# Kernel optimization log

Measured on AMD Instinct MI355X. Metric: run time of the kernel, lower is better.

## Reference

```python
import jax, jax.numpy as jnp
import numpy as np

N = 50000      # nodes
E = 1600000    # edges (before self loops)
F = 128        # input_dim
H = 4          # num_heads
D = 32         # hidden_dim (per head)
B = 16         # graphs in batch
NEG_SLOPE = 0.2  # PyG GATv2Conv default negative_slope


def setup_inputs() -> dict:
    key = jax.random.key(0)
    ks = jax.random.split(key, 8)
    x = jax.random.normal(ks[0], (N, F), dtype=jnp.float32)
    edge_index = jax.random.randint(ks[1], (2, E), 0, N, dtype=jnp.int32)
    batch = jnp.sort(jax.random.randint(ks[2], (N,), 0, B, dtype=jnp.int32))
    s = 0.05
    W_l = jax.random.normal(ks[3], (F, H * D), dtype=jnp.float32) * s
    b_l = jnp.zeros((H * D,), dtype=jnp.float32)
    W_r = jax.random.normal(ks[4], (F, H * D), dtype=jnp.float32) * s
    b_r = jnp.zeros((H * D,), dtype=jnp.float32)
    att = jax.random.normal(ks[5], (H, D), dtype=jnp.float32) * s
    bias = jnp.zeros((H * D,), dtype=jnp.float32)
    return {"x": x, "edge_index": edge_index, "batch": batch,
            "W_l": W_l, "b_l": b_l, "W_r": W_r, "b_r": b_r,
            "att": att, "bias": bias}


def reference(x, edge_index, batch, W_l, b_l, W_r, b_r, att, bias):
    n = x.shape[0]
    # PyG GATv2Conv adds self loops by default
    loops = jnp.arange(n, dtype=edge_index.dtype)
    src = jnp.concatenate([edge_index[0], loops])  # message source j
    dst = jnp.concatenate([edge_index[1], loops])  # message target i

    xl = (x @ W_l + b_l).reshape(n, H, D)  # source transform
    xr = (x @ W_r + b_r).reshape(n, H, D)  # target transform

    # per-edge GATv2 attention logits: a^T LeakyReLU(xl_j + xr_i)
    m = xl[src] + xr[dst]                                   # [E+N, H, D]
    e = jnp.sum(jax.nn.leaky_relu(m, NEG_SLOPE) * att, -1)  # [E+N, H]

    # softmax over incoming edges of each destination node
    e_max = jax.ops.segment_max(e, dst, num_segments=n)
    ex = jnp.exp(e - e_max[dst])
    den = jax.ops.segment_sum(ex, dst, num_segments=n)
    alpha = ex / den[dst]                                   # [E+N, H]

    # weighted scatter-sum aggregation of source features
    out = jax.ops.segment_sum(alpha[..., None] * xl[src], dst, num_segments=n)
    out = out.reshape(n, H * D) + bias                      # concat heads + bias
    out = jax.nn.relu(out)

    # global max pool over nodes of each graph
    pooled = jax.ops.segment_max(out, batch, num_segments=B)
    pooled = jnp.where(jnp.isfinite(pooled), pooled, 0.0)   # guard empty graphs
    return pooled
```

## Files before the change

kernel.cpp:

```cpp
#include <hip/hip_runtime.h>

#define NN 50000
#define NE 1600000
#define FDIM 128
#define CDIM 128
#define NGRAPH 16
#define SLOPE 0.2f
#define CSTRIDE 96
#define BINSH 7
#define NBIN 391
#define EPB 6400
#define NB1 250
#define EPT 25
#define CAP 5120
#define POOL_NODES 64
#define POOL_NB ((NN + POOL_NODES - 1) / POOL_NODES)
#define TNB 782

__device__ __forceinline__ unsigned short f2bf(float f) {
    unsigned u = __float_as_uint(f);
    return (unsigned short)((u + 0x7FFFu + ((u >> 16) & 1u)) >> 16);
}
__device__ __forceinline__ unsigned packbf(float a, float b) {
    return (unsigned)f2bf(a) | ((unsigned)f2bf(b) << 16);
}
#define BFLO(u) __uint_as_float((u) << 16)
#define BFHI(u) __uint_as_float((u) & 0xffff0000u)

typedef __attribute__((ext_vector_type(8))) short short8;
typedef __attribute__((ext_vector_type(4))) float f32x4;
union FragU { uint4 u; short8 s; };

__global__ __launch_bounds__(256) void k_init(float* __restrict__ out,
                                              int* __restrict__ gbin_cnt) {
    int i = blockIdx.x * 256 + threadIdx.x;
    if (i < NGRAPH * CDIM) out[i] = 0.f;
    if (i < NBIN) gbin_cnt[i] = 0;
}

__global__ __launch_bounds__(256) void k_transform(
    const float* __restrict__ x,
    const float* __restrict__ Wl, const float* __restrict__ bl,
    const float* __restrict__ Wr, const float* __restrict__ br,
    unsigned short* __restrict__ xlh, float* __restrict__ xr) {
    __shared__ uint4 wfrag[2048];
    const int tid   = threadIdx.x;
    const int wv    = tid >> 6;
    const int lane  = tid & 63;
    const int quad  = lane >> 4;
    const int col   = lane & 15;
    const int node0 = blockIdx.x * 64;
    const int nodeA = node0 + wv * 16 + col;
    const bool aval = nodeA < NN;

    FragU afrag[4];
#pragma unroll
    for (int kq = 0; kq < 4; kq++) {
        float4 lo = make_float4(0.f,0.f,0.f,0.f), hi = lo;
        if (aval) {
            const float* ap = &x[(size_t)nodeA * FDIM + kq * 32 + quad * 8];
            lo = *(const float4*)ap;
            hi = *(const float4*)(ap + 4);
        }
        afrag[kq].u.x = packbf(lo.x, lo.y);
        afrag[kq].u.y = packbf(lo.z, lo.w);
        afrag[kq].u.z = packbf(hi.x, hi.y);
        afrag[kq].u.w = packbf(hi.z, hi.w);
    }

    const int myrow0 = node0 + wv * 16 + quad * 4;

    for (int mat = 0; mat < 2; mat++) {
        const float* W  = mat ? Wr : Wl;
        const float* bb = mat ? br : bl;
        __syncthreads();
        for (int i = 0; i < 8; i++) {
            int C = i * 256 + tid;
            int ccol = C & 15, cq = (C >> 4) & 3, ckq = (C >> 6) & 3, cnt_ = C >> 8;
            const float* wp = &W[(size_t)(ckq * 32 + cq * 8) * CDIM + cnt_ * 16 + ccol];
            uint4 u;
            u.x = packbf(wp[0],        wp[CDIM]);
            u.y = packbf(wp[2*CDIM],   wp[3*CDIM]);
            u.z = packbf(wp[4*CDIM],   wp[5*CDIM]);
            u.w = packbf(wp[6*CDIM],   wp[7*CDIM]);
            wfrag[C] = u;
        }
        __syncthreads();

#pragma unroll
        for (int nt = 0; nt < 8; nt++) {
            f32x4 acc = {0.f, 0.f, 0.f, 0.f};
#pragma unroll
            for (int kq = 0; kq < 4; kq++) {
                FragU bfr;
                bfr.u = wfrag[(nt * 4 + kq) * 64 + lane];
                acc = __builtin_amdgcn_mfma_f32_16x16x32_bf16(
                          afrag[kq].s, bfr.s, acc, 0, 0, 0);
            }
            int ch = nt * 16 + col;
            float bv = bb[ch];
            if (mat == 0) {
#pragma unroll
                for (int r = 0; r < 4; r++) {
                    int node = myrow0 + r;
                    if (node < NN)
                        xlh[(size_t)node * CDIM + ch] = f2bf(acc[r] + bv);
                }
            } else {
#pragma unroll
                for (int r = 0; r < 4; r++) {
                    int node = myrow0 + r;
                    if (node < NN)
                        xr[(size_t)node * CDIM + ch] = acc[r] + bv;
                }
            }
        }
    }
}

__global__ __launch_bounds__(256) void k_bin(
    const int* __restrict__ src, const int* __restrict__ dst,
    int* __restrict__ gbin_cnt, unsigned* __restrict__ gstage) {
    __shared__ int bcnt[NBIN];
    __shared__ int boff[NBIN];
    __shared__ int gb[NBIN];
    __shared__ int sc[256];
    __shared__ unsigned st[EPB];
    const int t  = threadIdx.x;
    const int e0 = blockIdx.x * EPB;

    for (int b = t; b < NBIN; b += 256) bcnt[b] = 0;
    __syncthreads();

    unsigned sd[EPT]; int bn[EPT]; int pl[EPT];
#pragma unroll
    for (int k = 0; k < EPT; k++) {
        int e = e0 + k * 256 + t;
        int s = src[e], d = dst[e];
        bn[k] = d >> BINSH;
        sd[k] = (unsigned)s | ((unsigned)(d & 127) << 16)
                            | ((unsigned)bn[k] << 23);
        pl[k] = atomicAdd(&bcnt[bn[k]], 1);
    }
    __syncthreads();

    int c0 = (2*t     < NBIN) ? bcnt[2*t]     : 0;
    int c1 = (2*t + 1 < NBIN) ? bcnt[2*t + 1] : 0;
    int v  = c0 + c1;
    sc[t] = v; __syncthreads();
    for (int off = 1; off < 256; off <<= 1) {
        int add = (t >= off) ? sc[t - off] : 0;
        __syncthreads();
        sc[t] += add;
        __syncthreads();
    }
    int base = sc[t] - v;
    if (2*t     < NBIN) boff[2*t]     = base;
    if (2*t + 1 < NBIN) boff[2*t + 1] = base + c0;
    __syncthreads();

    for (int b = t; b < NBIN; b += 256) {
        int c = bcnt[b];
        gb[b] = (c > 0) ? atomicAdd(&gbin_cnt[b], c) : 0;
    }
#pragma unroll
    for (int k = 0; k < EPT; k++) st[boff[bn[k]] + pl[k]] = sd[k];
    __syncthreads();

    for (int idx = t; idx < EPB; idx += 256) {
        unsigned w = st[idx];
        int b = w >> 23;
        int p = gb[b] + (idx - boff[b]);
        if (p < CAP) gstage[(size_t)b * CAP + p] = w;
    }
}

__global__ __launch_bounds__(256) void k_csr(
    const int* __restrict__ gbin_cnt, const unsigned* __restrict__ gstage,
    int* __restrict__ cnt, unsigned short* __restrict__ colp) {
    __shared__ int nfill[128];
    __shared__ unsigned short crow[128 * CSTRIDE];
    const int bin = blockIdx.x;
    const int t   = threadIdx.x;
    const int n0  = bin << BINSH;
    const int nb  = min(128, NN - n0);
    const int m   = min(gbin_cnt[bin], CAP);

    if (t < 128) nfill[t] = 0;
    __syncthreads();

    for (int i = t; i < m; i += 256) {
        unsigned w = gstage[(size_t)bin * CAP + i];
        int dl = (w >> 16) & 127;
        int p  = atomicAdd(&nfill[dl], 1);
        if (p < CSTRIDE - 1) crow[dl * CSTRIDE + p] = (unsigned short)(w & 0xFFFF);
    }
    __syncthreads();

    if (t < nb) {
        int c = min(nfill[t], CSTRIDE - 1);
        crow[t * CSTRIDE + c] = (unsigned short)(n0 + t);
        cnt[n0 + t] = c + 1;
    }
    __syncthreads();

    unsigned* gout = (unsigned*)colp + (size_t)bin * (128 * CSTRIDE / 2);
    const unsigned* cin = (const unsigned*)crow;
    for (int idx = t; idx < 128 * CSTRIDE / 2; idx += 256) gout[idx] = cin[idx];
}

__global__ __launch_bounds__(256) void k_aggregate(
    const unsigned short* __restrict__ xlh, const float* __restrict__ xr,
    const float* __restrict__ att, const float* __restrict__ bias,
    const int* __restrict__ cnt, const unsigned short* __restrict__ colp,
    float* __restrict__ nodeout) {
    const int wave = blockIdx.x * 4 + (threadIdx.x >> 6);
    const int lane = threadIdx.x & 63;
    if (wave >= NN) return;
    const int i     = wave;
    const size_t start = (size_t)i * CSTRIDE;
    const int deg   = cnt[i];
    const int grp   = lane >> 4;
    const int sub   = lane & 15;
    const int ch0   = sub * 8;

    const float4 rx0 = *(const float4*)&xr[(size_t)i * CDIM + ch0];
    const float4 rx1 = *(const float4*)&xr[(size_t)i * CDIM + ch0 + 4];
    const float4 aa0 = *(const float4*)&att[ch0];
    const float4 aa1 = *(const float4*)&att[ch0 + 4];
    const float4 p0 = make_float4(0.6f*aa0.x, 0.6f*aa0.y, 0.6f*aa0.z, 0.6f*aa0.w);
    const float4 p1 = make_float4(0.6f*aa1.x, 0.6f*aa1.y, 0.6f*aa1.z, 0.6f*aa1.w);
    const float4 q0 = make_float4(0.4f*aa0.x, 0.4f*aa0.y, 0.4f*aa0.z, 0.4f*aa0.w);
    const float4 q1 = make_float4(0.4f*aa1.x, 0.4f*aa1.y, 0.4f*aa1.z, 0.4f*aa1.w);

    float s = 0.f;
    float acc[8];
#pragma unroll
    for (int k = 0; k < 8; k++) acc[k] = 0.f;

    for (int base = 0; base < deg; base += 64) {
        int rem = deg - base;
        int cnt64 = rem < 64 ? rem : 64;
        int cj  = (lane < cnt64) ? (int)colp[start + base + lane] : 0;
        int iters = (cnt64 + 3) >> 2;
        for (int t = 0; t < iters; t++) {
            int e = t * 4 + grp;
            int j = __shfl(cj, e);
            if (e < cnt64) {
                uint4 q = *(const uint4*)&xlh[(size_t)j * CDIM + ch0];
                float4 v0 = make_float4(BFLO(q.x), BFHI(q.x),
                                        BFLO(q.y), BFHI(q.y));
                float4 v1 = make_float4(BFLO(q.z), BFHI(q.z),
                                        BFLO(q.w), BFHI(q.w));
                float t0, d = 0.f;
                t0 = v0.x + rx0.x; d = fmaf(t0, p0.x, d); d = fmaf(fabsf(t0), q0.x, d);
                t0 = v0.y + rx0.y; d = fmaf(t0, p0.y, d); d = fmaf(fabsf(t0), q0.y, d);
                t0 = v0.z + rx0.z; d = fmaf(t0, p0.z, d); d = fmaf(fabsf(t0), q0.z, d);
                t0 = v0.w + rx0.w; d = fmaf(t0, p0.w, d); d = fmaf(fabsf(t0), q0.w, d);
                t0 = v1.x + rx1.x; d = fmaf(t0, p1.x, d); d = fmaf(fabsf(t0), q1.x, d);
                t0 = v1.y + rx1.y; d = fmaf(t0, p1.y, d); d = fmaf(fabsf(t0), q1.y, d);
                t0 = v1.z + rx1.z; d = fmaf(t0, p1.z, d); d = fmaf(fabsf(t0), q1.z, d);
                t0 = v1.w + rx1.w; d = fmaf(t0, p1.w, d); d = fmaf(fabsf(t0), q1.w, d);
                d += __shfl_xor(d, 1);
                d += __shfl_xor(d, 2);
                float w = __expf(d);
                s += w;
                acc[0] = fmaf(w, v0.x, acc[0]);
                acc[1] = fmaf(w, v0.y, acc[1]);
                acc[2] = fmaf(w, v0.z, acc[2]);
                acc[3] = fmaf(w, v0.w, acc[3]);
                acc[4] = fmaf(w, v1.x, acc[4]);
                acc[5] = fmaf(w, v1.y, acc[5]);
                acc[6] = fmaf(w, v1.z, acc[6]);
                acc[7] = fmaf(w, v1.w, acc[7]);
            }
        }
    }

#pragma unroll
    for (int dist = 16; dist <= 32; dist <<= 1) {
        s += __shfl_xor(s, dist);
#pragma unroll
        for (int k = 0; k < 8; k++) acc[k] += __shfl_xor(acc[k], dist);
    }

    if (grp == 0) {
        float inv = 1.f / s;
        float4 o0, o1;
        const float4 b0 = *(const float4*)&bias[ch0];
        const float4 b1 = *(const float4*)&bias[ch0 + 4];
        o0.x = fmaxf(fmaf(acc[0], inv, b0.x), 0.f);
        o0.y = fmaxf(fmaf(acc[1], inv, b0.y), 0.f);
        o0.z = fmaxf(fmaf(acc[2], inv, b0.z), 0.f);
        o0.w = fmaxf(fmaf(acc[3], inv, b0.w), 0.f);
        o1.x = fmaxf(fmaf(acc[4], inv, b1.x), 0.f);
        o1.y = fmaxf(fmaf(acc[5], inv, b1.y), 0.f);
        o1.z = fmaxf(fmaf(acc[6], inv, b1.z), 0.f);
        o1.w = fmaxf(fmaf(acc[7], inv, b1.w), 0.f);
        float* op = &nodeout[(size_t)i * CDIM + ch0];
        *(float4*)op       = o0;
        *(float4*)(op + 4) = o1;
    }
}

__global__ __launch_bounds__(256) void k_pool(
    const float* __restrict__ nodeout, const int* __restrict__ batch,
    float* __restrict__ out) {
    const int tid  = threadIdx.x;
    const int c4   = (tid & 31) * 4;
    const int nl   = tid >> 5;
    const int base = blockIdx.x * POOL_NODES;
    float4 mx = make_float4(0.f, 0.f, 0.f, 0.f);
    int cur = -1;
#pragma unroll
    for (int k = 0; k < POOL_NODES / 8; k++) {
        int node = base + k * 8 + nl;
        if (node >= NN) break;
        int g = batch[node];
        if (g != cur) {
            if (cur >= 0) {
                int* op = (int*)&out[cur * CDIM + c4];
                if (mx.x > 0.f) atomicMax(op,     __float_as_int(mx.x));
                if (mx.y > 0.f) atomicMax(op + 1, __float_as_int(mx.y));
                if (mx.z > 0.f) atomicMax(op + 2, __float_as_int(mx.z));
                if (mx.w > 0.f) atomicMax(op + 3, __float_as_int(mx.w));
            }
            cur = g;
            mx = make_float4(0.f, 0.f, 0.f, 0.f);
        }
        float4 v = *(const float4*)&nodeout[(size_t)node * CDIM + c4];
        mx.x = fmaxf(mx.x, v.x);
        mx.y = fmaxf(mx.y, v.y);
        mx.z = fmaxf(mx.z, v.z);
        mx.w = fmaxf(mx.w, v.w);
    }
    if (cur >= 0) {
        int* op = (int*)&out[cur * CDIM + c4];
        if (mx.x > 0.f) atomicMax(op,     __float_as_int(mx.x));
        if (mx.y > 0.f) atomicMax(op + 1, __float_as_int(mx.y));
        if (mx.z > 0.f) atomicMax(op + 2, __float_as_int(mx.z));
        if (mx.w > 0.f) atomicMax(op + 3, __float_as_int(mx.w));
    }
}

extern "C" void kernel_launch(void* const* d_in, const int* in_sizes, int n_in,
                              void* d_out, int out_size, void* d_ws, size_t ws_size,
                              hipStream_t stream) {
    const float* x     = (const float*)d_in[0];
    const int*   ei    = (const int*)d_in[1];
    const int*   batch = (const int*)d_in[2];
    const float* Wl    = (const float*)d_in[3];
    const float* bl    = (const float*)d_in[4];
    const float* Wr    = (const float*)d_in[5];
    const float* br    = (const float*)d_in[6];
    const float* att   = (const float*)d_in[7];
    const float* bias  = (const float*)d_in[8];
    float* out = (float*)d_out;

    char* w = (char*)d_ws;
    float*          xr       = (float*)w;          w += (size_t)NN * CDIM * 4;
    float*          nodeout  = (float*)w;          w += (size_t)NN * CDIM * 4;
    unsigned short* xlh      = (unsigned short*)w; w += (size_t)NN * CDIM * 2;
    int*            cnt      = (int*)w;            w += (size_t)NN * 4;
    unsigned short* colp     = (unsigned short*)w; w += (size_t)NBIN * 128 * CSTRIDE * 2;
    unsigned*       gstage   = (unsigned*)w;       w += (size_t)NBIN * CAP * 4;
    int*            gbin_cnt = (int*)w;            w += (size_t)NBIN * 4;

    const int* src = ei;
    const int* dst = ei + NE;

    k_init<<<10, 256, 0, stream>>>(out, gbin_cnt);
    k_bin<<<NB1, 256, 0, stream>>>(src, dst, gbin_cnt, gstage);
    k_csr<<<NBIN, 256, 0, stream>>>(gbin_cnt, gstage, cnt, colp);
    k_transform<<<TNB, 256, 0, stream>>>(x, Wl, bl, Wr, br, xlh, xr);
    k_aggregate<<<NN / 4, 256, 0, stream>>>(xlh, xr, att, bias,
                                            cnt, colp, nodeout);
    k_pool<<<POOL_NB, 256, 0, stream>>>(nodeout, batch, out);
}
```

Before: 241.0 us.

## Fuse binning and transform kernels into one launch; pack aggregate math into float2

Merges the edge-binning kernel and the MFMA feature-transform kernel into a single launch, with block ranges choosing the role and a shared raw buffer. The independent phases can then overlap on the GPU and one launch gap is removed. The aggregate inner loop is rewritten with two-wide float vectors and the leaky-ReLU is expressed as t*a - 0.8*a*min(t,0), to enable packed FP32 instructions. The merged kernel's register and shared-memory usage is the maximum of both roles, which may lower occupancy for either part.

```diff
diff --git a/kernel.cpp b/kernel.cpp
--- a/kernel.cpp
+++ b/kernel.cpp
@@ -29,6 +29,7 @@
 
 typedef __attribute__((ext_vector_type(8))) short short8;
 typedef __attribute__((ext_vector_type(4))) float f32x4;
+typedef __attribute__((ext_vector_type(2))) float v2f;
 union FragU { uint4 u; short8 s; };
 
 __global__ __launch_bounds__(256) void k_init(float* __restrict__ out,
@@ -38,140 +39,143 @@
     if (i < NBIN) gbin_cnt[i] = 0;
 }
 
-__global__ __launch_bounds__(256) void k_transform(
+__global__ __launch_bounds__(256) void k_front(
     const float* __restrict__ x,
     const float* __restrict__ Wl, const float* __restrict__ bl,
     const float* __restrict__ Wr, const float* __restrict__ br,
+    const int* __restrict__ src, const int* __restrict__ dst,
+    int* __restrict__ gbin_cnt, unsigned* __restrict__ gstage,
     unsigned short* __restrict__ xlh, float* __restrict__ xr) {
-    __shared__ uint4 wfrag[2048];
-    const int tid   = threadIdx.x;
-    const int wv    = tid >> 6;
-    const int lane  = tid & 63;
-    const int quad  = lane >> 4;
-    const int col   = lane & 15;
-    const int node0 = blockIdx.x * 64;
-    const int nodeA = node0 + wv * 16 + col;
-    const bool aval = nodeA < NN;
-
-    FragU afrag[4];
-#pragma unroll
-    for (int kq = 0; kq < 4; kq++) {
-        float4 lo = make_float4(0.f,0.f,0.f,0.f), hi = lo;
-        if (aval) {
-            const float* ap = &x[(size_t)nodeA * FDIM + kq * 32 + quad * 8];
-            lo = *(const float4*)ap;
-            hi = *(const float4*)(ap + 4);
-        }
-        afrag[kq].u.x = packbf(lo.x, lo.y);
-        afrag[kq].u.y = packbf(lo.z, lo.w);
-        afrag[kq].u.z = packbf(hi.x, hi.y);
-        afrag[kq].u.w = packbf(hi.z, hi.w);
-    }
-
-    const int myrow0 = node0 + wv * 16 + quad * 4;
-
-    for (int mat = 0; mat < 2; mat++) {
-        const float* W  = mat ? Wr : Wl;
-        const float* bb = mat ? br : bl;
+    __shared__ __align__(16) char shraw[32768];
+    const int tid = threadIdx.x;
+
+    if (blockIdx.x < NB1) {
+        int* bcnt = (int*)shraw;
+        int* boff = bcnt + NBIN;
+        int* gb   = boff + NBIN;
+        int* sc   = gb + NBIN;
+        unsigned* st = (unsigned*)(sc + 256);
+        const int t  = tid;
+        const int e0 = blockIdx.x * EPB;
+
+        for (int b = t; b < NBIN; b += 256) bcnt[b] = 0;
         __syncthreads();
-        for (int i = 0; i < 8; i++) {
-            int C = i * 256 + tid;
-            int ccol = C & 15, cq = (C >> 4) & 3, ckq = (C >> 6) & 3, cnt_ = C >> 8;
-            const float* wp = &W[(size_t)(ckq * 32 + cq * 8) * CDIM + cnt_ * 16 + ccol];
-            uint4 u;
-            u.x = packbf(wp[0],        wp[CDIM]);
-            u.y = packbf(wp[2*CDIM],   wp[3*CDIM]);
-            u.z = packbf(wp[4*CDIM],   wp[5*CDIM]);
-            u.w = packbf(wp[6*CDIM],   wp[7*CDIM]);
-            wfrag[C] = u;
+
+        unsigned sd[EPT]; int bn[EPT]; int pl[EPT];
+#pragma unroll
+        for (int k = 0; k < EPT; k++) {
+            int e = e0 + k * 256 + t;
+            int s = src[e], d = dst[e];
+            bn[k] = d >> BINSH;
+            sd[k] = (unsigned)s | ((unsigned)(d & 127) << 16)
+                                | ((unsigned)bn[k] << 23);
+            pl[k] = atomicAdd(&bcnt[bn[k]], 1);
         }
         __syncthreads();
 
-#pragma unroll
-        for (int nt = 0; nt < 8; nt++) {
-            f32x4 acc = {0.f, 0.f, 0.f, 0.f};
-#pragma unroll
-            for (int kq = 0; kq < 4; kq++) {
-                FragU bfr;
-                bfr.u = wfrag[(nt * 4 + kq) * 64 + lane];
-                acc = __builtin_amdgcn_mfma_f32_16x16x32_bf16(
-                          afrag[kq].s, bfr.s, acc, 0, 0, 0);
-            }
-            int ch = nt * 16 + col;
-            float bv = bb[ch];
-            if (mat == 0) {
-#pragma unroll
-                for (int r = 0; r < 4; r++) {
-                    int node = myrow0 + r;
-                    if (node < NN)
-                        xlh[(size_t)node * CDIM + ch] = f2bf(acc[r] + bv);
+        int c0 = (2*t     < NBIN) ? bcnt[2*t]     : 0;
+        int c1 = (2*t + 1 < NBIN) ? bcnt[2*t + 1] : 0;
+        int v  = c0 + c1;
+        sc[t] = v; __syncthreads();
+        for (int off = 1; off < 256; off <<= 1) {
+            int add = (t >= off) ? sc[t - off] : 0;
+            __syncthreads();
+            sc[t] += add;
+            __syncthreads();
+        }
+        int base = sc[t] - v;
+        if (2*t     < NBIN) boff[2*t]     = base;
+        if (2*t + 1 < NBIN) boff[2*t + 1] = base + c0;
+        __syncthreads();
+
+        for (int b = t; b < NBIN; b += 256) {
+            int c = bcnt[b];
+            gb[b] = (c > 0) ? atomicAdd(&gbin_cnt[b], c) : 0;
+        }
+#pragma unroll
+        for (int k = 0; k < EPT; k++) st[boff[bn[k]] + pl[k]] = sd[k];
+        __syncthreads();
+
+        for (int idx = t; idx < EPB; idx += 256) {
+            unsigned w = st[idx];
+            int b = w >> 23;
+            int p = gb[b] + (idx - boff[b]);
+            if (p < CAP) gstage[(size_t)b * CAP + p] = w;
+        }
+    } else {
+        uint4* wfrag = (uint4*)shraw;
+        const int bid   = blockIdx.x - NB1;
+        const int wv    = tid >> 6;
+        const int lane  = tid & 63;
+        const int quad  = lane >> 4;
+        const int col   = lane & 15;
+        const int node0 = bid * 64;
+        const int nodeA = node0 + wv * 16 + col;
+        const bool aval = nodeA < NN;
+
+        FragU afrag[4];
+#pragma unroll
+        for (int kq = 0; kq < 4; kq++) {
+            float4 lo = make_float4(0.f,0.f,0.f,0.f), hi = lo;
+            if (aval) {
+                const float* ap = &x[(size_t)nodeA * FDIM + kq * 32 + quad * 8];
+                lo = *(const float4*)ap;
+                hi = *(const float4*)(ap + 4);
+            }
+            afrag[kq].u.x = packbf(lo.x, lo.y);
+            afrag[kq].u.y = packbf(lo.z, lo.w);
+            afrag[kq].u.z = packbf(hi.x, hi.y);
+            afrag[kq].u.w = packbf(hi.z, hi.w);
+        }
+
+        const int myrow0 = node0 + wv * 16 + quad * 4;
+
+        for (int mat = 0; mat < 2; mat++) {
+            const float* W  = mat ? Wr : Wl;
+            const float* bb = mat ? br : bl;
+            __syncthreads();
+            for (int i = 0; i < 8; i++) {
+                int C = i * 256 + tid;
+                int ccol = C & 15, cq = (C >> 4) & 3, ckq = (C >> 6) & 3, cnt_ = C >> 8;
+                const float* wp = &W[(size_t)(ckq * 32 + cq * 8) * CDIM + cnt_ * 16 + ccol];
+                uint4 u;
+                u.x = packbf(wp[0],        wp[CDIM]);
+                u.y = packbf(wp[2*CDIM],   wp[3*CDIM]);
+                u.z = packbf(wp[4*CDIM],   wp[5*CDIM]);
+                u.w = packbf(wp[6*CDIM],   wp[7*CDIM]);
+                wfrag[C] = u;
+            }
+            __syncthreads();
+
+#pragma unroll
+            for (int nt = 0; nt < 8; nt++) {
+                f32x4 acc = {0.f, 0.f, 0.f, 0.f};
+#pragma unroll
+                for (int kq = 0; kq < 4; kq++) {
+                    FragU bfr;
+                    bfr.u = wfrag[(nt * 4 + kq) * 64 + lane];
+                    acc = __builtin_amdgcn_mfma_f32_16x16x32_bf16(
+                              afrag[kq].s, bfr.s, acc, 0, 0, 0);
                 }
-            } else {
-#pragma unroll
-                for (int r = 0; r < 4; r++) {
-                    int node = myrow0 + r;
-                    if (node < NN)
-                        xr[(size_t)node * CDIM + ch] = acc[r] + bv;
+                int ch = nt * 16 + col;
+                float bv = bb[ch];
+                if (mat == 0) {
+#pragma unroll
+                    for (int r = 0; r < 4; r++) {
+                        int node = myrow0 + r;
+                        if (node < NN)
+                            xlh[(size_t)node * CDIM + ch] = f2bf(acc[r] + bv);
+                    }
+                } else {
+#pragma unroll
+                    for (int r = 0; r < 4; r++) {
+                        int node = myrow0 + r;
+                        if (node < NN)
+                            xr[(size_t)node * CDIM + ch] = acc[r] + bv;
+                    }
                 }
             }
         }
-    }
-}
-
-__global__ __launch_bounds__(256) void k_bin(
-    const int* __restrict__ src, const int* __restrict__ dst,
-    int* __restrict__ gbin_cnt, unsigned* __restrict__ gstage) {
-    __shared__ int bcnt[NBIN];
-    __shared__ int boff[NBIN];
-    __shared__ int gb[NBIN];
-    __shared__ int sc[256];
-    __shared__ unsigned st[EPB];
-    const int t  = threadIdx.x;
-    const int e0 = blockIdx.x * EPB;
-
-    for (int b = t; b < NBIN; b += 256) bcnt[b] = 0;
-    __syncthreads();
-
-    unsigned sd[EPT]; int bn[EPT]; int pl[EPT];
-#pragma unroll
-    for (int k = 0; k < EPT; k++) {
-        int e = e0 + k * 256 + t;
-        int s = src[e], d = dst[e];
-        bn[k] = d >> BINSH;
-        sd[k] = (unsigned)s | ((unsigned)(d & 127) << 16)
-                            | ((unsigned)bn[k] << 23);
-        pl[k] = atomicAdd(&bcnt[bn[k]], 1);
-    }
-    __syncthreads();
-
-    int c0 = (2*t     < NBIN) ? bcnt[2*t]     : 0;
-    int c1 = (2*t + 1 < NBIN) ? bcnt[2*t + 1] : 0;
-    int v  = c0 + c1;
-    sc[t] = v; __syncthreads();
-    for (int off = 1; off < 256; off <<= 1) {
-        int add = (t >= off) ? sc[t - off] : 0;
-        __syncthreads();
-        sc[t] += add;
-        __syncthreads();
-    }
-    int base = sc[t] - v;
-    if (2*t     < NBIN) boff[2*t]     = base;
-    if (2*t + 1 < NBIN) boff[2*t + 1] = base + c0;
-    __syncthreads();
-
-    for (int b = t; b < NBIN; b += 256) {
-        int c = bcnt[b];
-        gb[b] = (c > 0) ? atomicAdd(&gbin_cnt[b], c) : 0;
-    }
-#pragma unroll
-    for (int k = 0; k < EPT; k++) st[boff[bn[k]] + pl[k]] = sd[k];
-    __syncthreads();
-
-    for (int idx = t; idx < EPB; idx += 256) {
-        unsigned w = st[idx];
-        int b = w >> 23;
-        int p = gb[b] + (idx - boff[b]);
-        if (p < CAP) gstage[(size_t)b * CAP + p] = w;
     }
 }
 
@@ -224,19 +228,20 @@
     const int sub   = lane & 15;
     const int ch0   = sub * 8;
 
-    const float4 rx0 = *(const float4*)&xr[(size_t)i * CDIM + ch0];
-    const float4 rx1 = *(const float4*)&xr[(size_t)i * CDIM + ch0 + 4];
-    const float4 aa0 = *(const float4*)&att[ch0];
-    const float4 aa1 = *(const float4*)&att[ch0 + 4];
-    const float4 p0 = make_float4(0.6f*aa0.x, 0.6f*aa0.y, 0.6f*aa0.z, 0.6f*aa0.w);
-    const float4 p1 = make_float4(0.6f*aa1.x, 0.6f*aa1.y, 0.6f*aa1.z, 0.6f*aa1.w);
-    const float4 q0 = make_float4(0.4f*aa0.x, 0.4f*aa0.y, 0.4f*aa0.z, 0.4f*aa0.w);
-    const float4 q1 = make_float4(0.4f*aa1.x, 0.4f*aa1.y, 0.4f*aa1.z, 0.4f*aa1.w);
+    v2f rx[4], pa[4], qa[4];
+#pragma unroll
+    for (int p = 0; p < 4; p++) {
+        rx[p] = *(const v2f*)&xr[(size_t)i * CDIM + ch0 + 2 * p];
+        v2f a = *(const v2f*)&att[ch0 + 2 * p];
+        pa[p] = a;
+        qa[p] = -0.8f * a;
+    }
 
     float s = 0.f;
-    float acc[8];
-#pragma unroll
-    for (int k = 0; k < 8; k++) acc[k] = 0.f;
+    v2f acc2[4];
+#pragma unroll
+    for (int p = 0; p < 4; p++) acc2[p] = 0.f;
+    const v2f vzero = 0.f;
 
     for (int base = 0; base < deg; base += 64) {
         int rem = deg - base;
@@ -248,34 +253,34 @@
             int j = __shfl(cj, e);
             if (e < cnt64) {
                 uint4 q = *(const uint4*)&xlh[(size_t)j * CDIM + ch0];
-                float4 v0 = make_float4(BFLO(q.x), BFHI(q.x),
-                                        BFLO(q.y), BFHI(q.y));
-                float4 v1 = make_float4(BFLO(q.z), BFHI(q.z),
-                                        BFLO(q.w), BFHI(q.w));
-                float t0, d = 0.f;
-                t0 = v0.x + rx0.x; d = fmaf(t0, p0.x, d); d = fmaf(fabsf(t0), q0.x, d);
-                t0 = v0.y + rx0.y; d = fmaf(t0, p0.y, d); d = fmaf(fabsf(t0), q0.y, d);
-                t0 = v0.z + rx0.z; d = fmaf(t0, p0.z, d); d = fmaf(fabsf(t0), q0.z, d);
-                t0 = v0.w + rx0.w; d = fmaf(t0, p0.w, d); d = fmaf(fabsf(t0), q0.w, d);
-                t0 = v1.x + rx1.x; d = fmaf(t0, p1.x, d); d = fmaf(fabsf(t0), q1.x, d);
-                t0 = v1.y + rx1.y; d = fmaf(t0, p1.y, d); d = fmaf(fabsf(t0), q1.y, d);
-                t0 = v1.z + rx1.z; d = fmaf(t0, p1.z, d); d = fmaf(fabsf(t0), q1.z, d);
-                t0 = v1.w + rx1.w; d = fmaf(t0, p1.w, d); d = fmaf(fabsf(t0), q1.w, d);
+                v2f v[4];
+                v[0] = (v2f){BFLO(q.x), BFHI(q.x)};
+                v[1] = (v2f){BFLO(q.y), BFHI(q.y)};
+                v[2] = (v2f){BFLO(q.z), BFHI(q.z)};
+                v[3] = (v2f){BFLO(q.w), BFHI(q.w)};
+                v2f d2 = 0.f;
+#pragma unroll
+                for (int p = 0; p < 4; p++) {
+                    v2f tt = v[p] + rx[p];
+                    d2 += tt * pa[p];
+                    v2f mn = __builtin_elementwise_min(tt, vzero);
+                    d2 += mn * qa[p];
+                }
+                float d = d2.x + d2.y;
                 d += __shfl_xor(d, 1);
                 d += __shfl_xor(d, 2);
                 float w = __expf(d);
                 s += w;
-                acc[0] = fmaf(w, v0.x, acc[0]);
-                acc[1] = fmaf(w, v0.y, acc[1]);
-                acc[2] = fmaf(w, v0.z, acc[2]);
-                acc[3] = fmaf(w, v0.w, acc[3]);
-                acc[4] = fmaf(w, v1.x, acc[4]);
-                acc[5] = fmaf(w, v1.y, acc[5]);
-                acc[6] = fmaf(w, v1.z, acc[6]);
-                acc[7] = fmaf(w, v1.w, acc[7]);
-            }
-        }
-    }
+                v2f w2 = {w, w};
+#pragma unroll
+                for (int p = 0; p < 4; p++) acc2[p] += w2 * v[p];
+            }
+        }
+    }
+
+    float acc[8];
+#pragma unroll
+    for (int p = 0; p < 4; p++) { acc[2*p] = acc2[p].x; acc[2*p+1] = acc2[p].y; }
 
 #pragma unroll
     for (int dist = 16; dist <= 32; dist <<= 1) {
@@ -370,9 +375,9 @@
     const int* dst = ei + NE;
 
     k_init<<<10, 256, 0, stream>>>(out, gbin_cnt);
-    k_bin<<<NB1, 256, 0, stream>>>(src, dst, gbin_cnt, gstage);
+    k_front<<<NB1 + TNB, 256, 0, stream>>>(x, Wl, bl, Wr, br,
+                                           src, dst, gbin_cnt, gstage, xlh, xr);
     k_csr<<<NBIN, 256, 0, stream>>>(gbin_cnt, gstage, cnt, colp);
-    k_transform<<<TNB, 256, 0, stream>>>(x, Wl, bl, Wr, br, xlh, xr);
     k_aggregate<<<NN / 4, 256, 0, stream>>>(xlh, xr, att, bias,
                                             cnt, colp, nodeout);
     k_pool<<<POOL_NB, 256, 0, stream>>>(nodeout, batch, out);
```

Result: slower. 246.6 us (+2.3%).

## Merge edge binning and node transform into one launch; restructure aggregate edge loop

Applied to the files above, without the earlier changes.

Fuses the edge-binning kernel and the MFMA node transform into a single kernel whose blocks branch on blockIdx. The two independent stages then share one launch and can run concurrently on the GPU. Separately, the aggregate kernel now preloads up to 128 neighbour indices up front and walks full groups of four edges without a per-iteration bound check, handling the leftover edges in one tail step. The fused kernel uses a 32KB shared buffer for both roles, which may lower occupancy for the transform blocks. The aggregate path assumes degree is at most 128, which CSTRIDE guarantees.

```diff
diff --git a/kernel.cpp b/kernel.cpp
--- a/kernel.cpp
+++ b/kernel.cpp
@@ -38,140 +38,143 @@
     if (i < NBIN) gbin_cnt[i] = 0;
 }
 
-__global__ __launch_bounds__(256) void k_transform(
+__global__ __launch_bounds__(256) void k_front(
     const float* __restrict__ x,
     const float* __restrict__ Wl, const float* __restrict__ bl,
     const float* __restrict__ Wr, const float* __restrict__ br,
+    const int* __restrict__ src, const int* __restrict__ dst,
+    int* __restrict__ gbin_cnt, unsigned* __restrict__ gstage,
     unsigned short* __restrict__ xlh, float* __restrict__ xr) {
-    __shared__ uint4 wfrag[2048];
-    const int tid   = threadIdx.x;
-    const int wv    = tid >> 6;
-    const int lane  = tid & 63;
-    const int quad  = lane >> 4;
-    const int col   = lane & 15;
-    const int node0 = blockIdx.x * 64;
-    const int nodeA = node0 + wv * 16 + col;
-    const bool aval = nodeA < NN;
-
-    FragU afrag[4];
-#pragma unroll
-    for (int kq = 0; kq < 4; kq++) {
-        float4 lo = make_float4(0.f,0.f,0.f,0.f), hi = lo;
-        if (aval) {
-            const float* ap = &x[(size_t)nodeA * FDIM + kq * 32 + quad * 8];
-            lo = *(const float4*)ap;
-            hi = *(const float4*)(ap + 4);
-        }
-        afrag[kq].u.x = packbf(lo.x, lo.y);
-        afrag[kq].u.y = packbf(lo.z, lo.w);
-        afrag[kq].u.z = packbf(hi.x, hi.y);
-        afrag[kq].u.w = packbf(hi.z, hi.w);
-    }
-
-    const int myrow0 = node0 + wv * 16 + quad * 4;
-
-    for (int mat = 0; mat < 2; mat++) {
-        const float* W  = mat ? Wr : Wl;
-        const float* bb = mat ? br : bl;
+    __shared__ __align__(16) char shraw[32768];
+    const int tid = threadIdx.x;
+
+    if (blockIdx.x < NB1) {
+        int* bcnt = (int*)shraw;
+        int* boff = bcnt + NBIN;
+        int* gb   = boff + NBIN;
+        int* sc   = gb + NBIN;
+        unsigned* st = (unsigned*)(sc + 256);
+        const int t  = tid;
+        const int e0 = blockIdx.x * EPB;
+
+        for (int b = t; b < NBIN; b += 256) bcnt[b] = 0;
         __syncthreads();
-        for (int i = 0; i < 8; i++) {
-            int C = i * 256 + tid;
-            int ccol = C & 15, cq = (C >> 4) & 3, ckq = (C >> 6) & 3, cnt_ = C >> 8;
-            const float* wp = &W[(size_t)(ckq * 32 + cq * 8) * CDIM + cnt_ * 16 + ccol];
-            uint4 u;
-            u.x = packbf(wp[0],        wp[CDIM]);
-            u.y = packbf(wp[2*CDIM],   wp[3*CDIM]);
-            u.z = packbf(wp[4*CDIM],   wp[5*CDIM]);
-            u.w = packbf(wp[6*CDIM],   wp[7*CDIM]);
-            wfrag[C] = u;
+
+        unsigned sd[EPT]; int bn[EPT]; int pl[EPT];
+#pragma unroll
+        for (int k = 0; k < EPT; k++) {
+            int e = e0 + k * 256 + t;
+            int s = src[e], d = dst[e];
+            bn[k] = d >> BINSH;
+            sd[k] = (unsigned)s | ((unsigned)(d & 127) << 16)
+                                | ((unsigned)bn[k] << 23);
+            pl[k] = atomicAdd(&bcnt[bn[k]], 1);
         }
         __syncthreads();
 
-#pragma unroll
-        for (int nt = 0; nt < 8; nt++) {
-            f32x4 acc = {0.f, 0.f, 0.f, 0.f};
-#pragma unroll
-            for (int kq = 0; kq < 4; kq++) {
-                FragU bfr;
-                bfr.u = wfrag[(nt * 4 + kq) * 64 + lane];
-                acc = __builtin_amdgcn_mfma_f32_16x16x32_bf16(
-                          afrag[kq].s, bfr.s, acc, 0, 0, 0);
+        int c0 = (2*t     < NBIN) ? bcnt[2*t]     : 0;
+        int c1 = (2*t + 1 < NBIN) ? bcnt[2*t + 1] : 0;
+        int v  = c0 + c1;
+        sc[t] = v; __syncthreads();
+        for (int off = 1; off < 256; off <<= 1) {
+            int add = (t >= off) ? sc[t - off] : 0;
+            __syncthreads();
+            sc[t] += add;
+            __syncthreads();
+        }
+        int base = sc[t] - v;
+        if (2*t     < NBIN) boff[2*t]     = base;
+        if (2*t + 1 < NBIN) boff[2*t + 1] = base + c0;
+        __syncthreads();
+
+        for (int b = t; b < NBIN; b += 256) {
+            int c = bcnt[b];
+            gb[b] = (c > 0) ? atomicAdd(&gbin_cnt[b], c) : 0;
+        }
+#pragma unroll
+        for (int k = 0; k < EPT; k++) st[boff[bn[k]] + pl[k]] = sd[k];
+        __syncthreads();
+
+        for (int idx = t; idx < EPB; idx += 256) {
+            unsigned w = st[idx];
+            int b = w >> 23;
+            int p = gb[b] + (idx - boff[b]);
+            if (p < CAP) gstage[(size_t)b * CAP + p] = w;
+        }
+    } else {
+        uint4* wfrag = (uint4*)shraw;
+        const int bid   = blockIdx.x - NB1;
+        const int wv    = tid >> 6;
+        const int lane  = tid & 63;
+        const int quad  = lane >> 4;
+        const int col   = lane & 15;
+        const int node0 = bid * 64;
+        const int nodeA = node0 + wv * 16 + col;
+        const bool aval = nodeA < NN;
+
+        FragU afrag[4];
+#pragma unroll
+        for (int kq = 0; kq < 4; kq++) {
+            float4 lo = make_float4(0.f,0.f,0.f,0.f), hi = lo;
+            if (aval) {
+                const float* ap = &x[(size_t)nodeA * FDIM + kq * 32 + quad * 8];
+                lo = *(const float4*)ap;
+                hi = *(const float4*)(ap + 4);
             }
-            int ch = nt * 16 + col;
-            float bv = bb[ch];
-            if (mat == 0) {
-#pragma unroll
-                for (int r = 0; r < 4; r++) {
-                    int node = myrow0 + r;
-                    if (node < NN)
-                        xlh[(size_t)node * CDIM + ch] = f2bf(acc[r] + bv);
+            afrag[kq].u.x = packbf(lo.x, lo.y);
+            afrag[kq].u.y = packbf(lo.z, lo.w);
+            afrag[kq].u.z = packbf(hi.x, hi.y);
+            afrag[kq].u.w = packbf(hi.z, hi.w);
+        }
+
+        const int myrow0 = node0 + wv * 16 + quad * 4;
+
+        for (int mat = 0; mat < 2; mat++) {
+            const float* W  = mat ? Wr : Wl;
+            const float* bb = mat ? br : bl;
+            __syncthreads();
+            for (int i = 0; i < 8; i++) {
+                int C = i * 256 + tid;
+                int ccol = C & 15, cq = (C >> 4) & 3, ckq = (C >> 6) & 3, cnt_ = C >> 8;
+                const float* wp = &W[(size_t)(ckq * 32 + cq * 8) * CDIM + cnt_ * 16 + ccol];
+                uint4 u;
+                u.x = packbf(wp[0],        wp[CDIM]);
+                u.y = packbf(wp[2*CDIM],   wp[3*CDIM]);
+                u.z = packbf(wp[4*CDIM],   wp[5*CDIM]);
+                u.w = packbf(wp[6*CDIM],   wp[7*CDIM]);
+                wfrag[C] = u;
+            }
+            __syncthreads();
+
+#pragma unroll
+            for (int nt = 0; nt < 8; nt++) {
+                f32x4 acc = {0.f, 0.f, 0.f, 0.f};
+#pragma unroll
+                for (int kq = 0; kq < 4; kq++) {
+                    FragU bfr;
+                    bfr.u = wfrag[(nt * 4 + kq) * 64 + lane];
+                    acc = __builtin_amdgcn_mfma_f32_16x16x32_bf16(
+                              afrag[kq].s, bfr.s, acc, 0, 0, 0);
                 }
-            } else {
-#pragma unroll
-                for (int r = 0; r < 4; r++) {
-                    int node = myrow0 + r;
-                    if (node < NN)
-                        xr[(size_t)node * CDIM + ch] = acc[r] + bv;
+                int ch = nt * 16 + col;
+                float bv = bb[ch];
+                if (mat == 0) {
+#pragma unroll
+                    for (int r = 0; r < 4; r++) {
+                        int node = myrow0 + r;
+                        if (node < NN)
+                            xlh[(size_t)node * CDIM + ch] = f2bf(acc[r] + bv);
+                    }
+                } else {
+#pragma unroll
+                    for (int r = 0; r < 4; r++) {
+                        int node = myrow0 + r;
+                        if (node < NN)
+                            xr[(size_t)node * CDIM + ch] = acc[r] + bv;
+                    }
                 }
             }
         }
-    }
-}
-
-__global__ __launch_bounds__(256) void k_bin(
-    const int* __restrict__ src, const int* __restrict__ dst,
-    int* __restrict__ gbin_cnt, unsigned* __restrict__ gstage) {
-    __shared__ int bcnt[NBIN];
-    __shared__ int boff[NBIN];
-    __shared__ int gb[NBIN];
-    __shared__ int sc[256];
-    __shared__ unsigned st[EPB];
-    const int t  = threadIdx.x;
-    const int e0 = blockIdx.x * EPB;
-
-    for (int b = t; b < NBIN; b += 256) bcnt[b] = 0;
-    __syncthreads();
-
-    unsigned sd[EPT]; int bn[EPT]; int pl[EPT];
-#pragma unroll
-    for (int k = 0; k < EPT; k++) {
-        int e = e0 + k * 256 + t;
-        int s = src[e], d = dst[e];
-        bn[k] = d >> BINSH;
-        sd[k] = (unsigned)s | ((unsigned)(d & 127) << 16)
-                            | ((unsigned)bn[k] << 23);
-        pl[k] = atomicAdd(&bcnt[bn[k]], 1);
-    }
-    __syncthreads();
-
-    int c0 = (2*t     < NBIN) ? bcnt[2*t]     : 0;
-    int c1 = (2*t + 1 < NBIN) ? bcnt[2*t + 1] : 0;
-    int v  = c0 + c1;
-    sc[t] = v; __syncthreads();
-    for (int off = 1; off < 256; off <<= 1) {
-        int add = (t >= off) ? sc[t - off] : 0;
-        __syncthreads();
-        sc[t] += add;
-        __syncthreads();
-    }
-    int base = sc[t] - v;
-    if (2*t     < NBIN) boff[2*t]     = base;
-    if (2*t + 1 < NBIN) boff[2*t + 1] = base + c0;
-    __syncthreads();
-
-    for (int b = t; b < NBIN; b += 256) {
-        int c = bcnt[b];
-        gb[b] = (c > 0) ? atomicAdd(&gbin_cnt[b], c) : 0;
-    }
-#pragma unroll
-    for (int k = 0; k < EPT; k++) st[boff[bn[k]] + pl[k]] = sd[k];
-    __syncthreads();
-
-    for (int idx = t; idx < EPB; idx += 256) {
-        unsigned w = st[idx];
-        int b = w >> 23;
-        int p = gb[b] + (idx - boff[b]);
-        if (p < CAP) gstage[(size_t)b * CAP + p] = w;
     }
 }
 
@@ -209,6 +212,38 @@
     for (int idx = t; idx < 128 * CSTRIDE / 2; idx += 256) gout[idx] = cin[idx];
 }
 
+__device__ __forceinline__ void edge_body(
+    const unsigned short* __restrict__ xlh, int j, int ch0,
+    const float4& rx0, const float4& rx1,
+    const float4& p0, const float4& p1,
+    const float4& q0, const float4& q1,
+    float& s, float* acc) {
+    uint4 q = *(const uint4*)&xlh[(size_t)j * CDIM + ch0];
+    float4 v0 = make_float4(BFLO(q.x), BFHI(q.x), BFLO(q.y), BFHI(q.y));
+    float4 v1 = make_float4(BFLO(q.z), BFHI(q.z), BFLO(q.w), BFHI(q.w));
+    float t0, d = 0.f;
+    t0 = v0.x + rx0.x; d = fmaf(t0, p0.x, d); d = fmaf(fabsf(t0), q0.x, d);
+    t0 = v0.y + rx0.y; d = fmaf(t0, p0.y, d); d = fmaf(fabsf(t0), q0.y, d);
+    t0 = v0.z + rx0.z; d = fmaf(t0, p0.z, d); d = fmaf(fabsf(t0), q0.z, d);
+    t0 = v0.w + rx0.w; d = fmaf(t0, p0.w, d); d = fmaf(fabsf(t0), q0.w, d);
+    t0 = v1.x + rx1.x; d = fmaf(t0, p1.x, d); d = fmaf(fabsf(t0), q1.x, d);
+    t0 = v1.y + rx1.y; d = fmaf(t0, p1.y, d); d = fmaf(fabsf(t0), q1.y, d);
+    t0 = v1.z + rx1.z; d = fmaf(t0, p1.z, d); d = fmaf(fabsf(t0), q1.z, d);
+    t0 = v1.w + rx1.w; d = fmaf(t0, p1.w, d); d = fmaf(fabsf(t0), q1.w, d);
+    d += __shfl_xor(d, 1);
+    d += __shfl_xor(d, 2);
+    float w = __expf(d);
+    s += w;
+    acc[0] = fmaf(w, v0.x, acc[0]);
+    acc[1] = fmaf(w, v0.y, acc[1]);
+    acc[2] = fmaf(w, v0.z, acc[2]);
+    acc[3] = fmaf(w, v0.w, acc[3]);
+    acc[4] = fmaf(w, v1.x, acc[4]);
+    acc[5] = fmaf(w, v1.y, acc[5]);
+    acc[6] = fmaf(w, v1.z, acc[6]);
+    acc[7] = fmaf(w, v1.w, acc[7]);
+}
+
 __global__ __launch_bounds__(256) void k_aggregate(
     const unsigned short* __restrict__ xlh, const float* __restrict__ xr,
     const float* __restrict__ att, const float* __restrict__ bias,
@@ -216,13 +251,15 @@
     float* __restrict__ nodeout) {
     const int wave = blockIdx.x * 4 + (threadIdx.x >> 6);
     const int lane = threadIdx.x & 63;
-    if (wave >= NN) return;
     const int i     = wave;
     const size_t start = (size_t)i * CSTRIDE;
     const int deg   = cnt[i];
     const int grp   = lane >> 4;
-    const int sub   = lane & 15;
-    const int ch0   = sub * 8;
+    const int ch0   = (lane & 15) * 8;
+
+    int cj0 = (int)colp[start + lane];
+    int cj1 = 0;
+    if (deg > 64) cj1 = (int)colp[start + 64 + lane];
 
     const float4 rx0 = *(const float4*)&xr[(size_t)i * CDIM + ch0];
     const float4 rx1 = *(const float4*)&xr[(size_t)i * CDIM + ch0 + 4];
@@ -238,44 +275,21 @@
 #pragma unroll
     for (int k = 0; k < 8; k++) acc[k] = 0.f;
 
-    for (int base = 0; base < deg; base += 64) {
-        int rem = deg - base;
-        int cnt64 = rem < 64 ? rem : 64;
-        int cj  = (lane < cnt64) ? (int)colp[start + base + lane] : 0;
-        int iters = (cnt64 + 3) >> 2;
-        for (int t = 0; t < iters; t++) {
-            int e = t * 4 + grp;
-            int j = __shfl(cj, e);
-            if (e < cnt64) {
-                uint4 q = *(const uint4*)&xlh[(size_t)j * CDIM + ch0];
-                float4 v0 = make_float4(BFLO(q.x), BFHI(q.x),
-                                        BFLO(q.y), BFHI(q.y));
-                float4 v1 = make_float4(BFLO(q.z), BFHI(q.z),
-                                        BFLO(q.w), BFHI(q.w));
-                float t0, d = 0.f;
-                t0 = v0.x + rx0.x; d = fmaf(t0, p0.x, d); d = fmaf(fabsf(t0), q0.x, d);
-                t0 = v0.y + rx0.y; d = fmaf(t0, p0.y, d); d = fmaf(fabsf(t0), q0.y, d);
-                t0 = v0.z + rx0.z; d = fmaf(t0, p0.z, d); d = fmaf(fabsf(t0), q0.z, d);
-                t0 = v0.w + rx0.w; d = fmaf(t0, p0.w, d); d = fmaf(fabsf(t0), q0.w, d);
-                t0 = v1.x + rx1.x; d = fmaf(t0, p1.x, d); d = fmaf(fabsf(t0), q1.x, d);
-                t0 = v1.y + rx1.y; d = fmaf(t0, p1.y, d); d = fmaf(fabsf(t0), q1.y, d);
-                t0 = v1.z + rx1.z; d = fmaf(t0, p1.z, d); d = fmaf(fabsf(t0), q1.z, d);
-                t0 = v1.w + rx1.w; d = fmaf(t0, p1.w, d); d = fmaf(fabsf(t0), q1.w, d);
-                d += __shfl_xor(d, 1);
-                d += __shfl_xor(d, 2);
-                float w = __expf(d);
-                s += w;
-                acc[0] = fmaf(w, v0.x, acc[0]);
-                acc[1] = fmaf(w, v0.y, acc[1]);
-                acc[2] = fmaf(w, v0.z, acc[2]);
-                acc[3] = fmaf(w, v0.w, acc[3]);
-                acc[4] = fmaf(w, v1.x, acc[4]);
-                acc[5] = fmaf(w, v1.y, acc[5]);
-                acc[6] = fmaf(w, v1.z, acc[6]);
-                acc[7] = fmaf(w, v1.w, acc[7]);
-            }
-        }
-    }
+    const int full = deg >> 2;
+    const int f0   = full < 16 ? full : 16;
+#pragma unroll 2
+    for (int t = 0; t < f0; t++) {
+        int j = __shfl(cj0, t * 4 + grp);
+        edge_body(xlh, j, ch0, rx0, rx1, p0, p1, q0, q1, s, acc);
+    }
+    for (int t = 16; t < full; t++) {
+        int j = __shfl(cj1, t * 4 + grp - 64);
+        edge_body(xlh, j, ch0, rx0, rx1, p0, p1, q0, q1, s, acc);
+    }
+    int e  = full * 4 + grp;
+    int jt = (e < 64) ? __shfl(cj0, e) : __shfl(cj1, (e - 64) & 63);
+    if (e < deg)
+        edge_body(xlh, jt, ch0, rx0, rx1, p0, p1, q0, q1, s, acc);
 
 #pragma unroll
     for (int dist = 16; dist <= 32; dist <<= 1) {
@@ -370,9 +384,9 @@
     const int* dst = ei + NE;
 
     k_init<<<10, 256, 0, stream>>>(out, gbin_cnt);
-    k_bin<<<NB1, 256, 0, stream>>>(src, dst, gbin_cnt, gstage);
+    k_front<<<NB1 + TNB, 256, 0, stream>>>(x, Wl, bl, Wr, br,
+                                           src, dst, gbin_cnt, gstage, xlh, xr);
     k_csr<<<NBIN, 256, 0, stream>>>(gbin_cnt, gstage, cnt, colp);
-    k_transform<<<TNB, 256, 0, stream>>>(x, Wl, bl, Wr, br, xlh, xr);
     k_aggregate<<<NN / 4, 256, 0, stream>>>(xlh, xr, att, bias,
                                             cnt, colp, nodeout);
     k_pool<<<POOL_NB, 256, 0, stream>>>(nodeout, batch, out);
```

New measurement: 237.3 us. Within noise of the previous version (-1.5%).
